# Performance work log

Measured on AMD Instinct MI355X. Metric: run time of the kernel, lower is better.

The kernel has to match this reference:

```python
import jax, jax.numpy as jnp
import numpy as np

N_USERS = 100_000
N_ENTITIES = 400_000
N_NODES = N_USERS + N_ENTITIES  # 500k
DIM = 64
N_EDGES = 2_000_000
BATCH = 4096
N_LAYERS = 3
CF_WEIGHT = 1.0
L2_REG = 1e-4


def setup_inputs() -> dict:
    key = jax.random.key(0)
    k_emb, k_e, k_u, k_p, k_n = jax.random.split(key, 5)
    # xavier_uniform on (N, D): bound = sqrt(6/(N+D))
    bound = float(np.sqrt(6.0 / (N_NODES + DIM)))
    emb = jax.random.uniform(k_emb, (N_NODES, DIM), jnp.float32, -bound, bound)
    edge_index = jax.random.randint(k_e, (2, N_EDGES), 0, N_NODES, dtype=jnp.int32)
    user_idx = jax.random.randint(k_u, (BATCH,), 0, N_USERS, dtype=jnp.int32)
    pos_item = jax.random.randint(k_p, (BATCH,), 0, N_NODES, dtype=jnp.int32)
    neg_item = jax.random.randint(k_n, (BATCH,), 0, N_NODES, dtype=jnp.int32)
    return {"emb": emb, "edge_index": edge_index, "user_idx": user_idx,
            "pos_item": pos_item, "neg_item": neg_item}


def _lightgcn(emb, edge_index, n_layers):
    # LGConv(normalize=True): x' = D^{-1/2} A D^{-1/2} x, no self loops.
    n = emb.shape[0]
    src, dst = edge_index[0], edge_index[1]
    deg = jax.ops.segment_sum(jnp.ones_like(dst, dtype=emb.dtype), dst,
                              num_segments=n)
    dinv = jnp.where(deg > 0, jax.lax.rsqrt(jnp.maximum(deg, 1e-12)), 0.0)
    norm = dinv[src] * dinv[dst]  # [E]
    x = emb
    acc = emb  # layer-0 term of the mean over stacked layers
    for _ in range(n_layers):
        msgs = x[src] * norm[:, None]  # [E, D] gather + scale
        x = jax.ops.segment_sum(msgs, dst, num_segments=n)  # scatter-add
        acc = acc + x
    return acc / (n_layers + 1)  # mean over (layers+1) stacked embeddings


def reference(emb, edge_index, user_idx, pos_item, neg_item):
    all_layer = _lightgcn(emb, edge_index, N_LAYERS)
    u = all_layer[user_idx]
    p = all_layer[pos_item]
    n_ = all_layer[neg_item]
    pos_score = jnp.sum(u * p, axis=-1)
    neg_score = jnp.sum(u * n_, axis=-1)
    # BPRLoss: -mean(logsigmoid(pos - neg)) == mean(softplus(neg - pos))
    cf_loss = jnp.mean(jax.nn.softplus(neg_score - pos_score))
    u_ego = emb[user_idx]
    p_ego = emb[pos_item]
    n_ego = emb[neg_item]
    reg_loss = 0.5 * (jnp.sum(u_ego ** 2) + jnp.sum(p_ego ** 2)
                      + jnp.sum(n_ego ** 2)) / float(BATCH)
    return CF_WEIGHT * cf_loss + L2_REG * reg_loss
```

## Files before the change

### kernel.cpp

```cpp
#include <hip/hip_runtime.h>
#include <cstdint>
#include <cstddef>

#define N_USERS   100000
#define N_NODES   500000
#define DIM       64
#define N_EDGES   2000000
#define BATCH     4096
#define SCAN_B    1024
#define NBLK      ((N_NODES + SCAN_B - 1) / SCAN_B)
#define X1C_CAP   350000
#define LA_CAP    150000
#define SCAT_BLK  ((N_EDGES / 8 + 255) / 256)
#define CONV_BLK  ((N_NODES * 16 + 255) / 256)
#define PROP_BLK  2048

typedef unsigned char uchar;
typedef unsigned short ushort;
typedef unsigned int uint;

__device__ __forceinline__ ushort f2bf(float f) {
    uint u = __float_as_uint(f);
    uint r = u + 0x7FFFu + ((u >> 16) & 1u);
    return (ushort)(r >> 16);
}
__device__ __forceinline__ float bflo(uint u) { return __uint_as_float(u << 16); }
__device__ __forceinline__ float bfhi(uint u) { return __uint_as_float(u & 0xFFFF0000u); }

__global__ void k_mark(const int* __restrict__ u, const int* __restrict__ p,
                       const int* __restrict__ n, uchar* __restrict__ f3,
                       uchar* __restrict__ fA, uchar* __restrict__ fB) {
    int i = blockIdx.x * blockDim.x + threadIdx.x;
    if (i >= 3 * BATCH) return;
    int idx;
    if (i < BATCH)          idx = u[i];
    else if (i < 2 * BATCH) idx = p[i - BATCH];
    else                    idx = n[i - 2 * BATCH];
    f3[idx] = 1; fA[idx] = 1; fB[idx] = 1;
}

__global__ void k_degexp(const int* __restrict__ src, const int* __restrict__ dst,
                         int* __restrict__ deg, const uchar* __restrict__ f3,
                         uchar* __restrict__ fA) {
    int t = blockIdx.x * blockDim.x + threadIdx.x;
    if (t < N_EDGES / 8) {
        int4 s0 = ((const int4*)src)[2 * t];
        int4 s1 = ((const int4*)src)[2 * t + 1];
        int4 d0 = ((const int4*)dst)[2 * t];
        int4 d1 = ((const int4*)dst)[2 * t + 1];
        atomicAdd(&deg[d0.x], 1); atomicAdd(&deg[d0.y], 1);
        atomicAdd(&deg[d0.z], 1); atomicAdd(&deg[d0.w], 1);
        atomicAdd(&deg[d1.x], 1); atomicAdd(&deg[d1.y], 1);
        atomicAdd(&deg[d1.z], 1); atomicAdd(&deg[d1.w], 1);
        if (f3[d0.x] && !fA[s0.x]) fA[s0.x] = 1;
        if (f3[d0.y] && !fA[s0.y]) fA[s0.y] = 1;
        if (f3[d0.z] && !fA[s0.z]) fA[s0.z] = 1;
        if (f3[d0.w] && !fA[s0.w]) fA[s0.w] = 1;
        if (f3[d1.x] && !fA[s1.x]) fA[s1.x] = 1;
        if (f3[d1.y] && !fA[s1.y]) fA[s1.y] = 1;
        if (f3[d1.z] && !fA[s1.z]) fA[s1.z] = 1;
        if (f3[d1.w] && !fA[s1.w]) fA[s1.w] = 1;
    }
}

__global__ void k_expand(const int* __restrict__ src, const int* __restrict__ dst,
                         const uchar* __restrict__ fin, uchar* __restrict__ fout) {
    int t = blockIdx.x * blockDim.x + threadIdx.x;
    if (t < N_EDGES / 8) {
        int4 s0 = ((const int4*)src)[2 * t];
        int4 s1 = ((const int4*)src)[2 * t + 1];
        int4 d0 = ((const int4*)dst)[2 * t];
        int4 d1 = ((const int4*)dst)[2 * t + 1];
        if (fin[d0.x] && !fout[s0.x]) fout[s0.x] = 1;
        if (fin[d0.y] && !fout[s0.y]) fout[s0.y] = 1;
        if (fin[d0.z] && !fout[s0.z]) fout[s0.z] = 1;
        if (fin[d0.w] && !fout[s0.w]) fout[s0.w] = 1;
        if (fin[d1.x] && !fout[s1.x]) fout[s1.x] = 1;
        if (fin[d1.y] && !fout[s1.y]) fout[s1.y] = 1;
        if (fin[d1.z] && !fout[s1.z]) fout[s1.z] = 1;
        if (fin[d1.w] && !fout[s1.w]) fout[s1.w] = 1;
    }
}

__global__ void k_scanA(const int* __restrict__ deg, const uchar* __restrict__ fA,
                        const uchar* __restrict__ fB, int* __restrict__ bsumD,
                        int* __restrict__ bsumP) {
    __shared__ int sD[SCAN_B];
    __shared__ int sP[SCAN_B];
    int i = blockIdx.x * SCAN_B + threadIdx.x;
    int d = 0, pk = 0;
    if (i < N_NODES) { d = deg[i]; pk = (int)fA[i] | ((int)fB[i] << 16); }
    sD[threadIdx.x] = d; sP[threadIdx.x] = pk;
    __syncthreads();
    for (int off = SCAN_B / 2; off; off >>= 1) {
        if (threadIdx.x < off) {
            sD[threadIdx.x] += sD[threadIdx.x + off];
            sP[threadIdx.x] += sP[threadIdx.x + off];
        }
        __syncthreads();
    }
    if (threadIdx.x == 0) { bsumD[blockIdx.x] = sD[0]; bsumP[blockIdx.x] = sP[0]; }
}

__global__ void k_scanB(const int* __restrict__ bsumD, const int* __restrict__ bsumP,
                        int* __restrict__ boffD, int* __restrict__ boffA,
                        int* __restrict__ boffB, int* __restrict__ counts) {
    __shared__ int sD[512];
    __shared__ int sA[512];
    __shared__ int sB[512];
    int d = (threadIdx.x < NBLK) ? bsumD[threadIdx.x] : 0;
    int p = (threadIdx.x < NBLK) ? bsumP[threadIdx.x] : 0;
    int a = p & 0xFFFF, b = p >> 16;
    sD[threadIdx.x] = d; sA[threadIdx.x] = a; sB[threadIdx.x] = b;
    __syncthreads();
    for (int off = 1; off < 512; off <<= 1) {
        int tD = (threadIdx.x >= off) ? sD[threadIdx.x - off] : 0;
        int tA = (threadIdx.x >= off) ? sA[threadIdx.x - off] : 0;
        int tB = (threadIdx.x >= off) ? sB[threadIdx.x - off] : 0;
        __syncthreads();
        sD[threadIdx.x] += tD; sA[threadIdx.x] += tA; sB[threadIdx.x] += tB;
        __syncthreads();
    }
    if (threadIdx.x < NBLK) {
        boffD[threadIdx.x] = sD[threadIdx.x] - d;
        boffA[threadIdx.x] = sA[threadIdx.x] - a;
        boffB[threadIdx.x] = sB[threadIdx.x] - b;
    }
    if (threadIdx.x == 511) { counts[0] = sA[511]; counts[1] = sB[511]; }
}

__global__ void k_scanC(const int* __restrict__ deg, const uchar* __restrict__ fA,
                        const uchar* __restrict__ fB,
                        const int* __restrict__ boffD, const int* __restrict__ boffA,
                        const int* __restrict__ boffB,
                        int* __restrict__ rowstart, float* __restrict__ dinv,
                        int* __restrict__ mapA, int* __restrict__ mapB,
                        int4* __restrict__ listA4, int4* __restrict__ listB4) {
    __shared__ int sD[SCAN_B];
    __shared__ int sP[SCAN_B];
    int i = blockIdx.x * SCAN_B + threadIdx.x;
    int d = 0, a = 0, b = 0;
    if (i < N_NODES) { d = deg[i]; a = (int)fA[i]; b = (int)fB[i]; }
    sD[threadIdx.x] = d; sP[threadIdx.x] = a | (b << 16);
    __syncthreads();
    for (int off = 1; off < SCAN_B; off <<= 1) {
        int tD = (threadIdx.x >= off) ? sD[threadIdx.x - off] : 0;
        int tP = (threadIdx.x >= off) ? sP[threadIdx.x - off] : 0;
        __syncthreads();
        sD[threadIdx.x] += tD; sP[threadIdx.x] += tP;
        __syncthreads();
    }
    if (i < N_NODES) {
        int exD = sD[threadIdx.x] - d + boffD[blockIdx.x];
        int incP = sP[threadIdx.x];
        int exA = (incP & 0xFFFF) - a + boffA[blockIdx.x];
        int exB = (incP >> 16) - b + boffB[blockIdx.x];
        rowstart[i] = exD;
        float dv = (d > 0) ? rsqrtf((float)d) : 0.0f;
        dinv[i] = dv;
        mapA[i] = a ? exA : -1;
        mapB[i] = b ? exB : -1;
        int4 ent = make_int4(exD, exD + d, __float_as_int(dv), 0);
        if (a) listA4[exA] = ent;
        if (b) listB4[exB] = ent;
    }
}

__global__ void k_convscatter(const float* __restrict__ emb,
                              const float* __restrict__ dinv,
                              ushort* __restrict__ embs,
                              const int* __restrict__ src, const int* __restrict__ dst,
                              const uchar* __restrict__ fB,
                              int* __restrict__ rowstart, int* __restrict__ csr_src) {
    if (blockIdx.x < SCAT_BLK) {
        int t = blockIdx.x * blockDim.x + threadIdx.x;
        if (t < N_EDGES / 8) {
            int4 s0 = ((const int4*)src)[2 * t];
            int4 s1 = ((const int4*)src)[2 * t + 1];
            int4 d0 = ((const int4*)dst)[2 * t];
            int4 d1 = ((const int4*)dst)[2 * t + 1];
            if (fB[d0.x]) csr_src[atomicAdd(&rowstart[d0.x], 1)] = s0.x;
            if (fB[d0.y]) csr_src[atomicAdd(&rowstart[d0.y], 1)] = s0.y;
            if (fB[d0.z]) csr_src[atomicAdd(&rowstart[d0.z], 1)] = s0.z;
            if (fB[d0.w]) csr_src[atomicAdd(&rowstart[d0.w], 1)] = s0.w;
            if (fB[d1.x]) csr_src[atomicAdd(&rowstart[d1.x], 1)] = s1.x;
            if (fB[d1.y]) csr_src[atomicAdd(&rowstart[d1.y], 1)] = s1.y;
            if (fB[d1.z]) csr_src[atomicAdd(&rowstart[d1.z], 1)] = s1.z;
            if (fB[d1.w]) csr_src[atomicAdd(&rowstart[d1.w], 1)] = s1.w;
        }
    } else {
        int c = (blockIdx.x - SCAT_BLK) * blockDim.x + threadIdx.x;
        if (c < N_NODES * 16) {
            int row = c >> 4;
            float4 v = ((const float4*)emb)[c];
            float dv = dinv[row];
            uint2 o;
            o.x = (uint)f2bf(v.x * dv) | ((uint)f2bf(v.y * dv) << 16);
            o.y = (uint)f2bf(v.z * dv) | ((uint)f2bf(v.w * dv) << 16);
            ((uint2*)embs)[c] = o;
        }
    }
}

__global__ void k_prop1(const ushort* __restrict__ embs, const int4* __restrict__ listB4,
                        const int* __restrict__ counts, const int* __restrict__ csr_src,
                        ushort* __restrict__ x1c) {
    int lane = threadIdx.x & 63;
    int sub = lane >> 4, q = lane & 15;
    int wv = (blockIdx.x * blockDim.x + threadIdx.x) >> 6;
    int nw = (gridDim.x * blockDim.x) >> 6;
    int cnt = counts[1];
    for (; wv < cnt; wv += nw) {
        int4 nb = listB4[wv];
        float4 acc = {0.f, 0.f, 0.f, 0.f};
        for (int i = nb.x + sub; i < nb.y; i += 4) {
            int s = csr_src[i];
            uint2 u = *(const uint2*)(embs + (size_t)s * DIM + q * 4);
            acc.x += bflo(u.x); acc.y += bfhi(u.x);
            acc.z += bflo(u.y); acc.w += bfhi(u.y);
        }
        for (int off = 16; off <= 32; off <<= 1) {
            acc.x += __shfl_xor(acc.x, off, 64);
            acc.y += __shfl_xor(acc.y, off, 64);
            acc.z += __shfl_xor(acc.z, off, 64);
            acc.w += __shfl_xor(acc.w, off, 64);
        }
        if (sub == 0) {
            float dv = __int_as_float(nb.z);
            float d2 = dv * dv;
            uint2 o;
            o.x = (uint)f2bf(acc.x * d2) | ((uint)f2bf(acc.y * d2) << 16);
            o.y = (uint)f2bf(acc.z * d2) | ((uint)f2bf(acc.w * d2) << 16);
            *(uint2*)(x1c + (size_t)wv * DIM + q * 4) = o;
        }
    }
}

__global__ void k_prop2(const ushort* __restrict__ x1c, const int* __restrict__ mapB,
                        const int4* __restrict__ listA4, const int* __restrict__ counts,
                        const int* __restrict__ csr_src, ushort* __restrict__ x2c) {
    int lane = threadIdx.x & 63;
    int sub = lane >> 4, q = lane & 15;
    int wv = (blockIdx.x * blockDim.x + threadIdx.x) >> 6;
    int nw = (gridDim.x * blockDim.x) >> 6;
    int cnt = counts[0];
    for (; wv < cnt; wv += nw) {
        int4 nb = listA4[wv];
        float4 acc = {0.f, 0.f, 0.f, 0.f};
        for (int i = nb.x + sub; i < nb.y; i += 4) {
            int s = csr_src[i];
            int slot = mapB[s];
            uint2 u = *(const uint2*)(x1c + (size_t)slot * DIM + q * 4);
            acc.x += bflo(u.x); acc.y += bfhi(u.x);
            acc.z += bflo(u.y); acc.w += bfhi(u.y);
        }
        for (int off = 16; off <= 32; off <<= 1) {
            acc.x += __shfl_xor(acc.x, off, 64);
            acc.y += __shfl_xor(acc.y, off, 64);
            acc.z += __shfl_xor(acc.z, off, 64);
            acc.w += __shfl_xor(acc.w, off, 64);
        }
        if (sub == 0) {
            float dv = __int_as_float(nb.z);
            float d2 = dv * dv;
            uint2 o;
            o.x = (uint)f2bf(acc.x * d2) | ((uint)f2bf(acc.y * d2) << 16);
            o.y = (uint)f2bf(acc.z * d2) | ((uint)f2bf(acc.w * d2) << 16);
            *(uint2*)(x2c + (size_t)wv * DIM + q * 4) = o;
        }
    }
}

__device__ __forceinline__ float x3_row(const ushort* __restrict__ x2c,
                                        const int* __restrict__ mapA,
                                        const int* __restrict__ csr_src,
                                        const int4* __restrict__ listB4,
                                        const int* __restrict__ mapB,
                                        int t, int lane) {
    int4 nb = listB4[mapB[t]];
    float acc = 0.f;
    for (int i = nb.x; i < nb.y; ++i) {
        int s = csr_src[i];
        int slot = mapA[s];
        acc += __uint_as_float((uint)x2c[(size_t)slot * DIM + lane] << 16);
    }
    return acc * __int_as_float(nb.z);
}

__global__ void k_loss(const float* __restrict__ emb, const ushort* __restrict__ x1c,
                       const ushort* __restrict__ x2c,
                       const int* __restrict__ mapA, const int* __restrict__ mapB,
                       const int4* __restrict__ listB4, const int* __restrict__ csr_src,
                       const float* __restrict__ dinv,
                       const int* __restrict__ u, const int* __restrict__ p,
                       const int* __restrict__ n, float* __restrict__ out) {
    int lane = threadIdx.x & 63;
    int w = (blockIdx.x * blockDim.x + threadIdx.x) >> 6;
    if (w >= BATCH) return;
    int ui = u[w], pi = p[w], ni = n[w];
    float dvu = dinv[ui], dvp = dinv[pi], dvn = dinv[ni];
    float rdu = dvu > 0.f ? 1.f / dvu : 0.f;
    float rdp = dvp > 0.f ? 1.f / dvp : 0.f;
    float rdn = dvn > 0.f ? 1.f / dvn : 0.f;
    float ue = emb[(size_t)ui * DIM + lane];
    float pe = emb[(size_t)pi * DIM + lane];
    float ne = emb[(size_t)ni * DIM + lane];
    float u1 = __uint_as_float((uint)x1c[(size_t)mapB[ui] * DIM + lane] << 16) * rdu;
    float p1 = __uint_as_float((uint)x1c[(size_t)mapB[pi] * DIM + lane] << 16) * rdp;
    float n1 = __uint_as_float((uint)x1c[(size_t)mapB[ni] * DIM + lane] << 16) * rdn;
    float u2 = __uint_as_float((uint)x2c[(size_t)mapA[ui] * DIM + lane] << 16) * rdu;
    float p2 = __uint_as_float((uint)x2c[(size_t)mapA[pi] * DIM + lane] << 16) * rdp;
    float n2 = __uint_as_float((uint)x2c[(size_t)mapA[ni] * DIM + lane] << 16) * rdn;
    float u3 = x3_row(x2c, mapA, csr_src, listB4, mapB, ui, lane);
    float p3 = x3_row(x2c, mapA, csr_src, listB4, mapB, pi, lane);
    float n3 = x3_row(x2c, mapA, csr_src, listB4, mapB, ni, lane);
    float uall = 0.25f * (ue + u1 + u2 + u3);
    float pall = 0.25f * (pe + p1 + p2 + p3);
    float nall = 0.25f * (ne + n1 + n2 + n3);
    float pos = uall * pall;
    float neg = uall * nall;
    float sq  = ue * ue + pe * pe + ne * ne;
    for (int off = 32; off; off >>= 1) {
        pos += __shfl_xor(pos, off, 64);
        neg += __shfl_xor(neg, off, 64);
        sq  += __shfl_xor(sq,  off, 64);
    }
    if (lane == 0) {
        float z = neg - pos;
        float sp = fmaxf(z, 0.0f) + log1pf(expf(-fabsf(z)));
        float contrib = sp * (1.0f / BATCH) + 1e-4f * 0.5f * sq * (1.0f / BATCH);
        atomicAdd(out, contrib);
    }
}

extern "C" void kernel_launch(void* const* d_in, const int* in_sizes, int n_in,
                              void* d_out, int out_size, void* d_ws, size_t ws_size,
                              hipStream_t stream) {
    const float* emb  = (const float*)d_in[0];
    const int*   edge = (const int*)d_in[1];
    const int*   src  = edge;
    const int*   dst  = edge + N_EDGES;
    const int*   uidx = (const int*)d_in[2];
    const int*   pidx = (const int*)d_in[3];
    const int*   nidx = (const int*)d_in[4];
    float* out = (float*)d_out;

    char* w = (char*)d_ws;
    ushort* embs    = (ushort*)w;                w += (size_t)N_NODES * DIM * 2;
    ushort* x1c     = (ushort*)w;                w += (size_t)X1C_CAP * DIM * 2;
    ushort* x2c     = (ushort*)w;                w += (size_t)LA_CAP * DIM * 2;
    float*  dinv    = (float*)w;                 w += (size_t)N_NODES * 4;
    int*    rowstart= (int*)w;                   w += (size_t)N_NODES * 4;
    int*    csr_src = (int*)w;                   w += (size_t)N_EDGES * 4;
    int*    mapA    = (int*)w;                   w += (size_t)N_NODES * 4;
    int*    mapB    = (int*)w;                   w += (size_t)N_NODES * 4;
    int4*   listA4  = (int4*)w;                  w += (size_t)LA_CAP * 16;
    int4*   listB4  = (int4*)w;                  w += (size_t)X1C_CAP * 16;
    char*   zbase   = w;
    int*    deg     = (int*)w;                   w += (size_t)N_NODES * 4;
    uchar*  flags   = (uchar*)w;                 w += (size_t)3 * N_NODES;
    uchar*  f3 = flags;
    uchar*  fA = flags + N_NODES;
    uchar*  fB = flags + 2 * N_NODES;
    size_t  zbytes  = (size_t)(w - zbase);
    int*    bsumD   = (int*)w;                   w += (size_t)NBLK * 4;
    int*    boffD   = (int*)w;                   w += (size_t)NBLK * 4;
    int*    bsumP   = (int*)w;                   w += (size_t)NBLK * 4;
    int*    boffA   = (int*)w;                   w += (size_t)NBLK * 4;
    int*    boffB   = (int*)w;                   w += (size_t)NBLK * 4;
    int*    counts  = (int*)w;                   w += 16;

    hipMemsetAsync(zbase, 0, zbytes, stream);
    hipMemsetAsync(out, 0, 4, stream);

    k_mark<<<(3 * BATCH + 255) / 256, 256, 0, stream>>>(uidx, pidx, nidx, f3, fA, fB);
    k_degexp<<<(N_EDGES / 8 + 255) / 256, 256, 0, stream>>>(src, dst, deg, f3, fA);
    k_expand<<<(N_EDGES / 8 + 255) / 256, 256, 0, stream>>>(src, dst, fA, fB);

    k_scanA<<<NBLK, SCAN_B, 0, stream>>>(deg, fA, fB, bsumD, bsumP);
    k_scanB<<<1, 512, 0, stream>>>(bsumD, bsumP, boffD, boffA, boffB, counts);
    k_scanC<<<NBLK, SCAN_B, 0, stream>>>(deg, fA, fB, boffD, boffA, boffB,
                                         rowstart, dinv, mapA, mapB, listA4, listB4);

    k_convscatter<<<SCAT_BLK + CONV_BLK, 256, 0, stream>>>(
        emb, dinv, embs, src, dst, fB, rowstart, csr_src);

    k_prop1<<<PROP_BLK, 256, 0, stream>>>(embs, listB4, counts, csr_src, x1c);
    k_prop2<<<PROP_BLK, 256, 0, stream>>>(x1c, mapB, listA4, counts, csr_src, x2c);

    k_loss<<<(BATCH * 64 + 255) / 256, 256, 0, stream>>>(
        emb, x1c, x2c, mapA, mapB, listB4, csr_src, dinv, uidx, pidx, nidx, out);
}
```

Measured before the change: 477.3 us.

## Move bf16 conversion into degree kernel and apply dinv during propagation

The fp32-to-bf16 conversion of embeddings no longer depends on dinv, so it is fused into the degree and frontier kernel instead of the CSR scatter kernel. The source-side dinv scaling moves into prop1 as an extra gathered load per edge. Edge kernels now handle 4 edges per thread instead of 8. The aim is to overlap the conversion with the atomic-bound degree pass and shorten the chain before propagation, at the cost of one extra dinv gather per edge in prop1.

```diff
diff --git a/kernel.cpp b/kernel.cpp
--- a/kernel.cpp
+++ b/kernel.cpp
@@ -11,7 +11,7 @@
 #define NBLK      ((N_NODES + SCAN_B - 1) / SCAN_B)
 #define X1C_CAP   350000
 #define LA_CAP    150000
-#define SCAT_BLK  ((N_EDGES / 8 + 255) / 256)
+#define EDG4_BLK  ((N_EDGES / 4 + 255) / 256)
 #define CONV_BLK  ((N_NODES * 16 + 255) / 256)
 #define PROP_BLK  2048
 
@@ -39,46 +39,44 @@
     f3[idx] = 1; fA[idx] = 1; fB[idx] = 1;
 }
 
-__global__ void k_degexp(const int* __restrict__ src, const int* __restrict__ dst,
-                         int* __restrict__ deg, const uchar* __restrict__ f3,
-                         uchar* __restrict__ fA) {
-    int t = blockIdx.x * blockDim.x + threadIdx.x;
-    if (t < N_EDGES / 8) {
-        int4 s0 = ((const int4*)src)[2 * t];
-        int4 s1 = ((const int4*)src)[2 * t + 1];
-        int4 d0 = ((const int4*)dst)[2 * t];
-        int4 d1 = ((const int4*)dst)[2 * t + 1];
-        atomicAdd(&deg[d0.x], 1); atomicAdd(&deg[d0.y], 1);
-        atomicAdd(&deg[d0.z], 1); atomicAdd(&deg[d0.w], 1);
-        atomicAdd(&deg[d1.x], 1); atomicAdd(&deg[d1.y], 1);
-        atomicAdd(&deg[d1.z], 1); atomicAdd(&deg[d1.w], 1);
-        if (f3[d0.x] && !fA[s0.x]) fA[s0.x] = 1;
-        if (f3[d0.y] && !fA[s0.y]) fA[s0.y] = 1;
-        if (f3[d0.z] && !fA[s0.z]) fA[s0.z] = 1;
-        if (f3[d0.w] && !fA[s0.w]) fA[s0.w] = 1;
-        if (f3[d1.x] && !fA[s1.x]) fA[s1.x] = 1;
-        if (f3[d1.y] && !fA[s1.y]) fA[s1.y] = 1;
-        if (f3[d1.z] && !fA[s1.z]) fA[s1.z] = 1;
-        if (f3[d1.w] && !fA[s1.w]) fA[s1.w] = 1;
+__global__ void k_degconv(const int* __restrict__ src, const int* __restrict__ dst,
+                          int* __restrict__ deg, const uchar* __restrict__ f3,
+                          uchar* __restrict__ fA,
+                          const float* __restrict__ emb, ushort* __restrict__ embs) {
+    if (blockIdx.x < EDG4_BLK) {
+        int t = blockIdx.x * blockDim.x + threadIdx.x;
+        if (t < N_EDGES / 4) {
+            int4 s0 = ((const int4*)src)[t];
+            int4 d0 = ((const int4*)dst)[t];
+            atomicAdd(&deg[d0.x], 1); atomicAdd(&deg[d0.y], 1);
+            atomicAdd(&deg[d0.z], 1); atomicAdd(&deg[d0.w], 1);
+            if (f3[d0.x] && !fA[s0.x]) fA[s0.x] = 1;
+            if (f3[d0.y] && !fA[s0.y]) fA[s0.y] = 1;
+            if (f3[d0.z] && !fA[s0.z]) fA[s0.z] = 1;
+            if (f3[d0.w] && !fA[s0.w]) fA[s0.w] = 1;
+        }
+    } else {
+        int c = (blockIdx.x - EDG4_BLK) * blockDim.x + threadIdx.x;
+        if (c < N_NODES * 16) {
+            float4 v = ((const float4*)emb)[c];
+            uint2 o;
+            o.x = (uint)f2bf(v.x) | ((uint)f2bf(v.y) << 16);
+            o.y = (uint)f2bf(v.z) | ((uint)f2bf(v.w) << 16);
+            ((uint2*)embs)[c] = o;
+        }
     }
 }
 
 __global__ void k_expand(const int* __restrict__ src, const int* __restrict__ dst,
                          const uchar* __restrict__ fin, uchar* __restrict__ fout) {
     int t = blockIdx.x * blockDim.x + threadIdx.x;
-    if (t < N_EDGES / 8) {
-        int4 s0 = ((const int4*)src)[2 * t];
-        int4 s1 = ((const int4*)src)[2 * t + 1];
-        int4 d0 = ((const int4*)dst)[2 * t];
-        int4 d1 = ((const int4*)dst)[2 * t + 1];
+    if (t < N_EDGES / 4) {
+        int4 s0 = ((const int4*)src)[t];
+        int4 d0 = ((const int4*)dst)[t];
         if (fin[d0.x] && !fout[s0.x]) fout[s0.x] = 1;
         if (fin[d0.y] && !fout[s0.y]) fout[s0.y] = 1;
         if (fin[d0.z] && !fout[s0.z]) fout[s0.z] = 1;
         if (fin[d0.w] && !fout[s0.w]) fout[s0.w] = 1;
-        if (fin[d1.x] && !fout[s1.x]) fout[s1.x] = 1;
-        if (fin[d1.y] && !fout[s1.y]) fout[s1.y] = 1;
-        if (fin[d1.z] && !fout[s1.z]) fout[s1.z] = 1;
-        if (fin[d1.w] && !fout[s1.w]) fout[s1.w] = 1;
     }
 }
 
@@ -166,45 +164,23 @@
     }
 }
 
-__global__ void k_convscatter(const float* __restrict__ emb,
-                              const float* __restrict__ dinv,
-                              ushort* __restrict__ embs,
-                              const int* __restrict__ src, const int* __restrict__ dst,
-                              const uchar* __restrict__ fB,
-                              int* __restrict__ rowstart, int* __restrict__ csr_src) {
-    if (blockIdx.x < SCAT_BLK) {
-        int t = blockIdx.x * blockDim.x + threadIdx.x;
-        if (t < N_EDGES / 8) {
-            int4 s0 = ((const int4*)src)[2 * t];
-            int4 s1 = ((const int4*)src)[2 * t + 1];
-            int4 d0 = ((const int4*)dst)[2 * t];
-            int4 d1 = ((const int4*)dst)[2 * t + 1];
-            if (fB[d0.x]) csr_src[atomicAdd(&rowstart[d0.x], 1)] = s0.x;
-            if (fB[d0.y]) csr_src[atomicAdd(&rowstart[d0.y], 1)] = s0.y;
-            if (fB[d0.z]) csr_src[atomicAdd(&rowstart[d0.z], 1)] = s0.z;
-            if (fB[d0.w]) csr_src[atomicAdd(&rowstart[d0.w], 1)] = s0.w;
-            if (fB[d1.x]) csr_src[atomicAdd(&rowstart[d1.x], 1)] = s1.x;
-            if (fB[d1.y]) csr_src[atomicAdd(&rowstart[d1.y], 1)] = s1.y;
-            if (fB[d1.z]) csr_src[atomicAdd(&rowstart[d1.z], 1)] = s1.z;
-            if (fB[d1.w]) csr_src[atomicAdd(&rowstart[d1.w], 1)] = s1.w;
-        }
-    } else {
-        int c = (blockIdx.x - SCAT_BLK) * blockDim.x + threadIdx.x;
-        if (c < N_NODES * 16) {
-            int row = c >> 4;
-            float4 v = ((const float4*)emb)[c];
-            float dv = dinv[row];
-            uint2 o;
-            o.x = (uint)f2bf(v.x * dv) | ((uint)f2bf(v.y * dv) << 16);
-            o.y = (uint)f2bf(v.z * dv) | ((uint)f2bf(v.w * dv) << 16);
-            ((uint2*)embs)[c] = o;
-        }
+__global__ void k_scatter(const int* __restrict__ src, const int* __restrict__ dst,
+                          const uchar* __restrict__ fB, int* __restrict__ rowstart,
+                          int* __restrict__ csr_src) {
+    int t = blockIdx.x * blockDim.x + threadIdx.x;
+    if (t < N_EDGES / 4) {
+        int4 s0 = ((const int4*)src)[t];
+        int4 d0 = ((const int4*)dst)[t];
+        if (fB[d0.x]) csr_src[atomicAdd(&rowstart[d0.x], 1)] = s0.x;
+        if (fB[d0.y]) csr_src[atomicAdd(&rowstart[d0.y], 1)] = s0.y;
+        if (fB[d0.z]) csr_src[atomicAdd(&rowstart[d0.z], 1)] = s0.z;
+        if (fB[d0.w]) csr_src[atomicAdd(&rowstart[d0.w], 1)] = s0.w;
     }
 }
 
 __global__ void k_prop1(const ushort* __restrict__ embs, const int4* __restrict__ listB4,
                         const int* __restrict__ counts, const int* __restrict__ csr_src,
-                        ushort* __restrict__ x1c) {
+                        const float* __restrict__ dinv, ushort* __restrict__ x1c) {
     int lane = threadIdx.x & 63;
     int sub = lane >> 4, q = lane & 15;
     int wv = (blockIdx.x * blockDim.x + threadIdx.x) >> 6;
@@ -215,9 +191,12 @@
         float4 acc = {0.f, 0.f, 0.f, 0.f};
         for (int i = nb.x + sub; i < nb.y; i += 4) {
             int s = csr_src[i];
+            float dvs = dinv[s];
             uint2 u = *(const uint2*)(embs + (size_t)s * DIM + q * 4);
-            acc.x += bflo(u.x); acc.y += bfhi(u.x);
-            acc.z += bflo(u.y); acc.w += bfhi(u.y);
+            acc.x = fmaf(bflo(u.x), dvs, acc.x);
+            acc.y = fmaf(bfhi(u.x), dvs, acc.y);
+            acc.z = fmaf(bflo(u.y), dvs, acc.z);
+            acc.w = fmaf(bfhi(u.y), dvs, acc.w);
         }
         for (int off = 16; off <= 32; off <<= 1) {
             acc.x += __shfl_xor(acc.x, off, 64);
@@ -374,18 +353,20 @@
     hipMemsetAsync(out, 0, 4, stream);
 
     k_mark<<<(3 * BATCH + 255) / 256, 256, 0, stream>>>(uidx, pidx, nidx, f3, fA, fB);
-    k_degexp<<<(N_EDGES / 8 + 255) / 256, 256, 0, stream>>>(src, dst, deg, f3, fA);
-    k_expand<<<(N_EDGES / 8 + 255) / 256, 256, 0, stream>>>(src, dst, fA, fB);
+
+    k_degconv<<<EDG4_BLK + CONV_BLK, 256, 0, stream>>>(src, dst, deg, f3, fA,
+                                                       emb, embs);
+
+    k_expand<<<EDG4_BLK, 256, 0, stream>>>(src, dst, fA, fB);
 
     k_scanA<<<NBLK, SCAN_B, 0, stream>>>(deg, fA, fB, bsumD, bsumP);
     k_scanB<<<1, 512, 0, stream>>>(bsumD, bsumP, boffD, boffA, boffB, counts);
     k_scanC<<<NBLK, SCAN_B, 0, stream>>>(deg, fA, fB, boffD, boffA, boffB,
                                          rowstart, dinv, mapA, mapB, listA4, listB4);
 
-    k_convscatter<<<SCAT_BLK + CONV_BLK, 256, 0, stream>>>(
-        emb, dinv, embs, src, dst, fB, rowstart, csr_src);
-
-    k_prop1<<<PROP_BLK, 256, 0, stream>>>(embs, listB4, counts, csr_src, x1c);
+    k_scatter<<<EDG4_BLK, 256, 0, stream>>>(src, dst, fB, rowstart, csr_src);
+
+    k_prop1<<<PROP_BLK, 256, 0, stream>>>(embs, listB4, counts, csr_src, dinv, x1c);
     k_prop2<<<PROP_BLK, 256, 0, stream>>>(x1c, mapB, listA4, counts, csr_src, x2c);
 
     k_loss<<<(BATCH * 64 + 255) / 256, 256, 0, stream>>>(
```

Result: no change. 470.7 us (-1.4%).
